# Performance work log

Hardware: AMD Instinct MI355X
Metric: run time of the kernel (lower is better)

Reference implementation:

```python
import jax, jax.numpy as jnp
import numpy as np

N, F_IN, F_OUT = 8192, 256, 256
ALPHA = 0.2  # LeakyReLU negative slope
NEG = -9e15

def setup_inputs() -> dict:
    key = jax.random.key(0)
    k1, k2, k3, k4, k5 = jax.random.split(key, 5)
    h = jax.random.normal(k1, (N, F_IN), dtype=jnp.float32)
    adj = jax.random.randint(k2, (N, N), 0, 2, dtype=jnp.int32)
    W_w = jax.random.normal(k3, (F_IN, F_OUT), dtype=jnp.float32) / np.sqrt(F_IN)
    W_b = jax.random.normal(k4, (F_OUT,), dtype=jnp.float32) * 0.01
    a = jax.random.normal(k5, (2 * F_OUT, 1), dtype=jnp.float32) / np.sqrt(2 * F_OUT)
    return {"h": h, "adj": adj, "W_w": W_w, "W_b": W_b, "a": a}

def reference(h, adj, W_w, W_b, a):
    # Wh: [N, F_OUT]
    Wh = h @ W_w + W_b
    a1 = a[:F_OUT, 0]   # scores for source node i (row)
    a2 = a[F_OUT:, 0]   # scores for target node j (col)
    # e[i,j] = leakyrelu(Wh_i . a1 + Wh_j . a2)  -- separable form of the
    # original repeat/cat construction, identical math without the NxNx2F tensor.
    e = jax.nn.leaky_relu((Wh @ a1)[:, None] + (Wh @ a2)[None, :], negative_slope=ALPHA)
    attention = jnp.where(adj > 0, e, NEG)
    attention = jax.nn.softmax(attention, axis=1)
    # dropout is identity in eval / p=0
    h_prime = attention @ Wh  # [N, F_OUT]
    return h_prime
```

## Files before the change

### kernel.cpp

```cpp
#include <hip/hip_runtime.h>
#include <stdint.h>

#define NN 8192
#define FD 256
#define LOG2E 1.44269504088896340736f
#define SPLIT 8
#define JSLICE (NN / SPLIT)
#define NIT (JSLICE / 32)

typedef __attribute__((ext_vector_type(8))) __bf16 bf16x8;
typedef __attribute__((ext_vector_type(4))) float f32x4;

__device__ __forceinline__ unsigned short f2bf(float x) {
    unsigned u = __float_as_uint(x);
    u = u + 0x7fffu + ((u >> 16) & 1u);
    return (unsigned short)(u >> 16);
}
__device__ __forceinline__ bf16x8 ld_bf8(const unsigned short* p) {
    uint4 v = *(const uint4*)p;
    return __builtin_bit_cast(bf16x8, v);
}
__device__ __forceinline__ unsigned pack_trunc2(float a, float b) {
    return __builtin_amdgcn_perm(__float_as_uint(b), __float_as_uint(a), 0x07060302u);
}
__device__ __forceinline__ void async_ld16(const void* g, void* lds) {
    __builtin_amdgcn_global_load_lds(
        (const __attribute__((address_space(1))) void*)g,
        (__attribute__((address_space(3))) void*)lds, 16, 0, 0);
}

__global__ __launch_bounds__(256) void wtrans_kernel(const float* __restrict__ W,
                                                     unsigned short* __restrict__ WbT) {
    int idx = blockIdx.x * 256 + threadIdx.x;
    int k = idx >> 8, f = idx & 255;
    WbT[f * 256 + k] = f2bf(W[idx]);
}

__global__ __launch_bounds__(256) void adjpack_kernel(const int* __restrict__ adj,
                                                      unsigned* __restrict__ adjB) {
    int t = threadIdx.x;
    int l = t & 63, w = t >> 6;
    int i = blockIdx.x * 4 + w;
    const int* arow = adj + (size_t)i * NN;
    unsigned* brow = adjB + (size_t)i * (NN / 32);
    #pragma unroll 2
    for (int c = 0; c < 32; ++c) {
        int base = c * 256;
        int v0 = arow[base + l];
        int v1 = arow[base + 64 + l];
        int v2 = arow[base + 128 + l];
        int v3 = arow[base + 192 + l];
        unsigned long long b0 = __ballot(v0 > 0);
        unsigned long long b1 = __ballot(v1 > 0);
        unsigned long long b2 = __ballot(v2 > 0);
        unsigned long long b3 = __ballot(v3 > 0);
        if (l == 0) {
            uint4 lo = make_uint4((unsigned)b0, (unsigned)(b0 >> 32),
                                  (unsigned)b1, (unsigned)(b1 >> 32));
            uint4 hi = make_uint4((unsigned)b2, (unsigned)(b2 >> 32),
                                  (unsigned)b3, (unsigned)(b3 >> 32));
            *(uint4*)(brow + c * 8) = lo;
            *(uint4*)(brow + c * 8 + 4) = hi;
        }
    }
}

__global__ __launch_bounds__(256) void btrans_kernel(const unsigned* __restrict__ rm,
                                                     unsigned* __restrict__ tm) {
    __shared__ unsigned tile[64 * 65];
    int t = threadIdx.x;
    int l = t & 63, r0 = t >> 6;
    int i0 = (blockIdx.x & 127) * 64;
    int w0 = (blockIdx.x >> 7) * 64;
    #pragma unroll
    for (int k = 0; k < 16; ++k) {
        int r = k * 4 + r0;
        tile[r * 65 + l] = rm[(size_t)(i0 + r) * (NN / 32) + w0 + l];
    }
    __syncthreads();
    #pragma unroll
    for (int k = 0; k < 16; ++k) {
        int wi = k * 4 + r0;
        tm[(size_t)(w0 + wi) * NN + i0 + l] = tile[l * 65 + wi];
    }
}

__global__ __launch_bounds__(256) void gemm1_kernel(const float* __restrict__ h,
                                                    const unsigned short* __restrict__ WbT,
                                                    const float* __restrict__ bias,
                                                    const float* __restrict__ av,
                                                    unsigned short* __restrict__ PBu,
                                                    float* __restrict__ f1p,
                                                    float* __restrict__ f2p) {
    __shared__ float Wh_s[256 * 33];
    __shared__ float red_s[2 * 8 * 32];
    int t = threadIdx.x;
    int l = t & 63, w = t >> 6;
    int i0 = blockIdx.x * 32;
    int fbase = w * 64;
    int cl = l & 15, q = l >> 4;

    f32x4 acc[2][4] = {};
    const float* hA0 = h + (size_t)(i0 + cl) * FD;
    const float* hA1 = h + (size_t)(i0 + 16 + cl) * FD;

    #pragma unroll
    for (int ks = 0; ks < 8; ++ks) {
        int kk = ks * 32 + q * 8;
        union { unsigned short u[8]; bf16x8 v; } ua0, ua1;
        float4 x0 = *(const float4*)(hA0 + kk);
        float4 x1 = *(const float4*)(hA0 + kk + 4);
        float4 y0 = *(const float4*)(hA1 + kk);
        float4 y1 = *(const float4*)(hA1 + kk + 4);
        ua0.u[0]=f2bf(x0.x); ua0.u[1]=f2bf(x0.y); ua0.u[2]=f2bf(x0.z); ua0.u[3]=f2bf(x0.w);
        ua0.u[4]=f2bf(x1.x); ua0.u[5]=f2bf(x1.y); ua0.u[6]=f2bf(x1.z); ua0.u[7]=f2bf(x1.w);
        ua1.u[0]=f2bf(y0.x); ua1.u[1]=f2bf(y0.y); ua1.u[2]=f2bf(y0.z); ua1.u[3]=f2bf(y0.w);
        ua1.u[4]=f2bf(y1.x); ua1.u[5]=f2bf(y1.y); ua1.u[6]=f2bf(y1.z); ua1.u[7]=f2bf(y1.w);
        #pragma unroll
        for (int bg = 0; bg < 4; ++bg) {
            bf16x8 bF = ld_bf8(WbT + (fbase + bg * 16 + cl) * 256 + kk);
            acc[0][bg] = __builtin_amdgcn_mfma_f32_16x16x32_bf16(ua0.v, bF, acc[0][bg], 0, 0, 0);
            acc[1][bg] = __builtin_amdgcn_mfma_f32_16x16x32_bf16(ua1.v, bF, acc[1][bg], 0, 0, 0);
        }
    }

    #pragma unroll
    for (int mt = 0; mt < 2; ++mt)
        #pragma unroll
        for (int bg = 0; bg < 4; ++bg)
            #pragma unroll
            for (int e = 0; e < 4; ++e) {
                int il = mt * 16 + q * 4 + e;
                int fl = fbase + bg * 16 + cl;
                Wh_s[fl * 33 + il] = acc[mt][bg][e] + bias[fl];
            }
    __syncthreads();
    {
        size_t jcBase = (size_t)blockIdx.x * 8192;
        #pragma unroll
        for (int u = 0; u < 4; ++u) {
            int fg = u * 4 + (t >> 6);
            int ll = t & 63;
            int c2 = ll & 15, q2 = ll >> 4;
            const float* src = &Wh_s[(fg * 16 + c2) * 33 + q2 * 8];
            union { unsigned short us[8]; uint4 v; } p;
            #pragma unroll
            for (int e = 0; e < 8; ++e) p.us[e] = f2bf(src[e]);
            *(uint4*)(PBu + jcBase + fg * 512 + ll * 8) = p.v;
        }
    }
    {
        int i = t & 31, fc = t >> 5;
        float s1 = 0.f, s2 = 0.f;
        #pragma unroll
        for (int fo = 0; fo < 32; ++fo) {
            int f = fc * 32 + fo;
            float wv = Wh_s[f * 33 + i];
            s1 += wv * av[f];
            s2 += wv * av[256 + f];
        }
        red_s[fc * 32 + i] = s1;
        red_s[256 + fc * 32 + i] = s2;
    }
    __syncthreads();
    if (t < 32) {
        float s = 0.f;
        #pragma unroll
        for (int fc = 0; fc < 8; ++fc) s += red_s[fc * 32 + t];
        f1p[i0 + t] = s * LOG2E;
    } else if (t < 64) {
        int i = t - 32;
        float s = 0.f;
        #pragma unroll
        for (int fc = 0; fc < 8; ++fc) s += red_s[256 + fc * 32 + i];
        f2p[i0 + i] = s * LOG2E;
    }
}

__global__ __launch_bounds__(256, 3) void gat_kernel(const unsigned* __restrict__ adjBT,
                                                     const unsigned short* __restrict__ PBu,
                                                     const float* __restrict__ f1p,
                                                     const float* __restrict__ f2p,
                                                     float* __restrict__ num,
                                                     float* __restrict__ den) {
    __shared__ __align__(16) unsigned short Bs[2][8192];
    __shared__ unsigned mask_s[NIT * 64];
    __shared__ float f2_s[JSLICE];

    int t = threadIdx.x;
    int l = t & 63, w = t >> 6;
    int s = blockIdx.x & 7;
    int strip = blockIdx.x >> 3;
    int i0b = strip * 64;
    int j0 = s * JSLICE;
    int jw0 = j0 / 32;
    int cl = l & 15, q = l >> 4;

    #pragma unroll
    for (int c = 0; c < 8; ++c) {
        int idx = c * 256 + t;
        int jt = idx >> 6, rl = idx & 63;
        mask_s[idx] = adjBT[(size_t)(jw0 + jt) * NN + i0b + rl];
    }
    *(float4*)&f2_s[t * 4] = *(const float4*)(f2p + j0 + t * 4);

    const char* pbBase = (const char*)(PBu + (size_t)jw0 * 8192);
    #pragma unroll
    for (int k = 0; k < 4; ++k)
        async_ld16(pbBase + k * 4096 + t * 16, (char*)&Bs[0][0] + k * 4096 + t * 16);

    float f1v = f1p[i0b + w * 16 + cl];

    const bf16x8 onesB = __builtin_bit_cast(bf16x8,
        make_uint4(0x3F803F80u, 0x3F803F80u, 0x3F803F80u, 0x3F803F80u));

    f32x4 acc[16] = {};
    f32x4 accR = {};

    #pragma unroll 1
    for (int g = 0; g < NIT; ++g) {
        __syncthreads();
        if (g + 1 < NIT) {
            const char* src = pbBase + (size_t)(g + 1) * 16384;
            char* dst = (char*)&Bs[(g + 1) & 1][0];
            #pragma unroll
            for (int k = 0; k < 4; ++k)
                async_ld16(src + k * 4096 + t * 16, dst + k * 4096 + t * 16);
        }
        unsigned mw = mask_s[g * 64 + w * 16 + cl];
        float4 F0 = *(const float4*)&f2_s[g * 32 + q * 8];
        float4 F1 = *(const float4*)&f2_s[g * 32 + q * 8 + 4];

        unsigned bits = mw >> (q * 8);
        float fe[8] = {F0.x, F0.y, F0.z, F0.w, F1.x, F1.y, F1.z, F1.w};
        float wv[8];
        #pragma unroll
        for (int e = 0; e < 8; ++e) {
            float sv = f1v + fe[e];
            sv = fmaxf(sv, 0.2f * sv);
            float x = __builtin_amdgcn_exp2f(sv);
            x = (bits >> e) & 1 ? x : 0.f;
            wv[e] = x;
        }
        union { unsigned uu[4]; bf16x8 v; } af;
        af.uu[0] = pack_trunc2(wv[0], wv[1]);
        af.uu[1] = pack_trunc2(wv[2], wv[3]);
        af.uu[2] = pack_trunc2(wv[4], wv[5]);
        af.uu[3] = pack_trunc2(wv[6], wv[7]);

        const unsigned short* bu = &Bs[g & 1][0] + l * 8;
        #pragma unroll
        for (int fg = 0; fg < 16; ++fg) {
            bf16x8 B = ld_bf8(bu + fg * 512);
            acc[fg] = __builtin_amdgcn_mfma_f32_16x16x32_bf16(af.v, B, acc[fg], 0, 0, 0);
        }
        accR = __builtin_amdgcn_mfma_f32_16x16x32_bf16(af.v, onesB, accR, 0, 0, 0);
    }

    if (cl == 0) {
        #pragma unroll
        for (int e = 0; e < 4; ++e)
            den[(size_t)s * NN + i0b + w * 16 + q * 4 + e] = accR[e];
    }

    float* nrow = num + (size_t)s * NN * FD;
    #pragma unroll
    for (int e = 0; e < 4; ++e) {
        int r = i0b + w * 16 + q * 4 + e;
        #pragma unroll
        for (int fg = 0; fg < 16; ++fg)
            nrow[(size_t)r * FD + fg * 16 + cl] = acc[fg][e];
    }
}

__global__ __launch_bounds__(256) void combine_kernel(const float* __restrict__ num,
                                                      const float* __restrict__ den,
                                                      float* __restrict__ out) {
    int idx = blockIdx.x * 256 + threadIdx.x;
    int i = idx >> 8;
    float nsum = 0.f, dsum = 0.f;
    #pragma unroll
    for (int s = 0; s < SPLIT; ++s) {
        nsum += num[(size_t)s * NN * FD + idx];
        dsum += den[(size_t)s * NN + i];
    }
    out[idx] = nsum / dsum;
}

extern "C" void kernel_launch(void* const* d_in, const int* in_sizes, int n_in,
                              void* d_out, int out_size, void* d_ws, size_t ws_size,
                              hipStream_t stream) {
    const float* h   = (const float*)d_in[0];
    const int*   adj = (const int*)d_in[1];
    const float* W   = (const float*)d_in[2];
    const float* b   = (const float*)d_in[3];
    const float* a   = (const float*)d_in[4];
    float* out = (float*)d_out;

    char* ws = (char*)d_ws;
    unsigned short* PBu = (unsigned short*)ws;
    unsigned short* WbT = (unsigned short*)(ws + (4u << 20));
    float* f1p = (float*)(ws + (4u << 20) + (128u << 10));
    float* f2p = f1p + NN;
    float* den = f2p + NN;
    unsigned* adjB  = (unsigned*)(ws + (8u << 20));
    unsigned* adjBT = (unsigned*)(ws + (16u << 20));
    float* num = (float*)(ws + (24u << 20));

    adjpack_kernel<<<NN / 4, 256, 0, stream>>>(adj, adjB);
    wtrans_kernel<<<256, 256, 0, stream>>>(W, WbT);
    btrans_kernel<<<512, 256, 0, stream>>>(adjB, adjBT);
    gemm1_kernel<<<256, 256, 0, stream>>>(h, WbT, b, a, PBu, f1p, f2p);
    gat_kernel<<<128 * SPLIT, 256, 0, stream>>>(adjBT, PBu, f1p, f2p, num, den);
    combine_kernel<<<NN * FD / 256, 256, 0, stream>>>(num, den, out);
}
```

Measured before the change: 460.9 us.

## Fuse adjacency bit-packing into GAT kernel with prefetched ballot masks

Removes the separate adjacency pack and bit-transpose kernels. The GAT kernel now reads the int32 adjacency rows directly, ballots them into per-iteration bitmasks, and double-buffers the masks in LDS while the next tile's adjacency loads overlap the MFMA work. It also raises the occupancy hint to 4 blocks and remaps gemm1's block index so its output chunks are produced in a different order. The intent is to drop the extra kernel launches and the intermediate bitmask traffic. The cost is that the 256MB adjacency read now sits inside the compute kernel and adds register pressure.

Measured after the change: 439.1 us. 1.05x faster.

```diff
diff --git a/kernel.cpp b/kernel.cpp
--- a/kernel.cpp
+++ b/kernel.cpp
@@ -34,55 +34,6 @@
     int idx = blockIdx.x * 256 + threadIdx.x;
     int k = idx >> 8, f = idx & 255;
     WbT[f * 256 + k] = f2bf(W[idx]);
-}
-
-__global__ __launch_bounds__(256) void adjpack_kernel(const int* __restrict__ adj,
-                                                      unsigned* __restrict__ adjB) {
-    int t = threadIdx.x;
-    int l = t & 63, w = t >> 6;
-    int i = blockIdx.x * 4 + w;
-    const int* arow = adj + (size_t)i * NN;
-    unsigned* brow = adjB + (size_t)i * (NN / 32);
-    #pragma unroll 2
-    for (int c = 0; c < 32; ++c) {
-        int base = c * 256;
-        int v0 = arow[base + l];
-        int v1 = arow[base + 64 + l];
-        int v2 = arow[base + 128 + l];
-        int v3 = arow[base + 192 + l];
-        unsigned long long b0 = __ballot(v0 > 0);
-        unsigned long long b1 = __ballot(v1 > 0);
-        unsigned long long b2 = __ballot(v2 > 0);
-        unsigned long long b3 = __ballot(v3 > 0);
-        if (l == 0) {
-            uint4 lo = make_uint4((unsigned)b0, (unsigned)(b0 >> 32),
-                                  (unsigned)b1, (unsigned)(b1 >> 32));
-            uint4 hi = make_uint4((unsigned)b2, (unsigned)(b2 >> 32),
-                                  (unsigned)b3, (unsigned)(b3 >> 32));
-            *(uint4*)(brow + c * 8) = lo;
-            *(uint4*)(brow + c * 8 + 4) = hi;
-        }
-    }
-}
-
-__global__ __launch_bounds__(256) void btrans_kernel(const unsigned* __restrict__ rm,
-                                                     unsigned* __restrict__ tm) {
-    __shared__ unsigned tile[64 * 65];
-    int t = threadIdx.x;
-    int l = t & 63, r0 = t >> 6;
-    int i0 = (blockIdx.x & 127) * 64;
-    int w0 = (blockIdx.x >> 7) * 64;
-    #pragma unroll
-    for (int k = 0; k < 16; ++k) {
-        int r = k * 4 + r0;
-        tile[r * 65 + l] = rm[(size_t)(i0 + r) * (NN / 32) + w0 + l];
-    }
-    __syncthreads();
-    #pragma unroll
-    for (int k = 0; k < 16; ++k) {
-        int wi = k * 4 + r0;
-        tm[(size_t)(w0 + wi) * NN + i0 + l] = tile[l * 65 + wi];
-    }
 }
 
 __global__ __launch_bounds__(256) void gemm1_kernel(const float* __restrict__ h,
@@ -96,7 +47,8 @@
     __shared__ float red_s[2 * 8 * 32];
     int t = threadIdx.x;
     int l = t & 63, w = t >> 6;
-    int i0 = blockIdx.x * 32;
+    int jc = (blockIdx.x & 7) * 32 + (blockIdx.x >> 3);
+    int i0 = jc * 32;
     int fbase = w * 64;
     int cl = l & 15, q = l >> 4;
 
@@ -136,7 +88,7 @@
             }
     __syncthreads();
     {
-        size_t jcBase = (size_t)blockIdx.x * 8192;
+        size_t jcBase = (size_t)jc * 8192;
         #pragma unroll
         for (int u = 0; u < 4; ++u) {
             int fg = u * 4 + (t >> 6);
@@ -177,14 +129,14 @@
     }
 }
 
-__global__ __launch_bounds__(256, 3) void gat_kernel(const unsigned* __restrict__ adjBT,
+__global__ __launch_bounds__(256, 4) void gat_kernel(const int* __restrict__ adj,
                                                      const unsigned short* __restrict__ PBu,
                                                      const float* __restrict__ f1p,
                                                      const float* __restrict__ f2p,
                                                      float* __restrict__ num,
                                                      float* __restrict__ den) {
     __shared__ __align__(16) unsigned short Bs[2][8192];
-    __shared__ unsigned mask_s[NIT * 64];
+    __shared__ unsigned mask_b[2][64];
     __shared__ float f2_s[JSLICE];
 
     int t = threadIdx.x;
@@ -196,18 +148,32 @@
     int jw0 = j0 / 32;
     int cl = l & 15, q = l >> 4;
 
-    #pragma unroll
-    for (int c = 0; c < 8; ++c) {
-        int idx = c * 256 + t;
-        int jt = idx >> 6, rl = idx & 63;
-        mask_s[idx] = adjBT[(size_t)(jw0 + jt) * NN + i0b + rl];
-    }
     *(float4*)&f2_s[t * 4] = *(const float4*)(f2p + j0 + t * 4);
 
     const char* pbBase = (const char*)(PBu + (size_t)jw0 * 8192);
     #pragma unroll
     for (int k = 0; k < 4; ++k)
         async_ld16(pbBase + k * 4096 + t * 16, (char*)&Bs[0][0] + k * 4096 + t * 16);
+
+    const int* arow = adj + (size_t)(i0b + w * 16 + (l >> 5)) * NN + j0 + (l & 31);
+    {
+        int v0 = arow[0 * 2 * NN], v1 = arow[1 * 2 * NN], v2 = arow[2 * 2 * NN], v3 = arow[3 * 2 * NN];
+        int v4 = arow[4 * 2 * NN], v5 = arow[5 * 2 * NN], v6 = arow[6 * 2 * NN], v7 = arow[7 * 2 * NN];
+        unsigned long long b0 = __ballot(v0 > 0), b1 = __ballot(v1 > 0);
+        unsigned long long b2 = __ballot(v2 > 0), b3 = __ballot(v3 > 0);
+        unsigned long long b4 = __ballot(v4 > 0), b5 = __ballot(v5 > 0);
+        unsigned long long b6 = __ballot(v6 > 0), b7 = __ballot(v7 > 0);
+        if (l == 0) {
+            *(uint2*)&mask_b[0][w * 16 + 0]  = make_uint2((unsigned)b0, (unsigned)(b0 >> 32));
+            *(uint2*)&mask_b[0][w * 16 + 2]  = make_uint2((unsigned)b1, (unsigned)(b1 >> 32));
+            *(uint2*)&mask_b[0][w * 16 + 4]  = make_uint2((unsigned)b2, (unsigned)(b2 >> 32));
+            *(uint2*)&mask_b[0][w * 16 + 6]  = make_uint2((unsigned)b3, (unsigned)(b3 >> 32));
+            *(uint2*)&mask_b[0][w * 16 + 8]  = make_uint2((unsigned)b4, (unsigned)(b4 >> 32));
+            *(uint2*)&mask_b[0][w * 16 + 10] = make_uint2((unsigned)b5, (unsigned)(b5 >> 32));
+            *(uint2*)&mask_b[0][w * 16 + 12] = make_uint2((unsigned)b6, (unsigned)(b6 >> 32));
+            *(uint2*)&mask_b[0][w * 16 + 14] = make_uint2((unsigned)b7, (unsigned)(b7 >> 32));
+        }
+    }
 
     float f1v = f1p[i0b + w * 16 + cl];
 
@@ -220,14 +186,21 @@
     #pragma unroll 1
     for (int g = 0; g < NIT; ++g) {
         __syncthreads();
+        int a0, a1, a2, a3, a4, a5, a6, a7;
         if (g + 1 < NIT) {
             const char* src = pbBase + (size_t)(g + 1) * 16384;
             char* dst = (char*)&Bs[(g + 1) & 1][0];
             #pragma unroll
             for (int k = 0; k < 4; ++k)
                 async_ld16(src + k * 4096 + t * 16, dst + k * 4096 + t * 16);
-        }
-        unsigned mw = mask_s[g * 64 + w * 16 + cl];
+            int jo = (g + 1) * 32;
+            a0 = arow[0 * 2 * NN + jo]; a1 = arow[1 * 2 * NN + jo];
+            a2 = arow[2 * 2 * NN + jo]; a3 = arow[3 * 2 * NN + jo];
+            a4 = arow[4 * 2 * NN + jo]; a5 = arow[5 * 2 * NN + jo];
+            a6 = arow[6 * 2 * NN + jo]; a7 = arow[7 * 2 * NN + jo];
+        }
+
+        unsigned mw = mask_b[g & 1][w * 16 + cl];
         float4 F0 = *(const float4*)&f2_s[g * 32 + q * 8];
         float4 F1 = *(const float4*)&f2_s[g * 32 + q * 8 + 4];
 
@@ -255,6 +228,24 @@
             acc[fg] = __builtin_amdgcn_mfma_f32_16x16x32_bf16(af.v, B, acc[fg], 0, 0, 0);
         }
         accR = __builtin_amdgcn_mfma_f32_16x16x32_bf16(af.v, onesB, accR, 0, 0, 0);
+
+        if (g + 1 < NIT) {
+            int nb = (g + 1) & 1;
+            unsigned long long b0 = __ballot(a0 > 0), b1 = __ballot(a1 > 0);
+            unsigned long long b2 = __ballot(a2 > 0), b3 = __ballot(a3 > 0);
+            unsigned long long b4 = __ballot(a4 > 0), b5 = __ballot(a5 > 0);
+            unsigned long long b6 = __ballot(a6 > 0), b7 = __ballot(a7 > 0);
+            if (l == 0) {
+                *(uint2*)&mask_b[nb][w * 16 + 0]  = make_uint2((unsigned)b0, (unsigned)(b0 >> 32));
+                *(uint2*)&mask_b[nb][w * 16 + 2]  = make_uint2((unsigned)b1, (unsigned)(b1 >> 32));
+                *(uint2*)&mask_b[nb][w * 16 + 4]  = make_uint2((unsigned)b2, (unsigned)(b2 >> 32));
+                *(uint2*)&mask_b[nb][w * 16 + 6]  = make_uint2((unsigned)b3, (unsigned)(b3 >> 32));
+                *(uint2*)&mask_b[nb][w * 16 + 8]  = make_uint2((unsigned)b4, (unsigned)(b4 >> 32));
+                *(uint2*)&mask_b[nb][w * 16 + 10] = make_uint2((unsigned)b5, (unsigned)(b5 >> 32));
+                *(uint2*)&mask_b[nb][w * 16 + 12] = make_uint2((unsigned)b6, (unsigned)(b6 >> 32));
+                *(uint2*)&mask_b[nb][w * 16 + 14] = make_uint2((unsigned)b7, (unsigned)(b7 >> 32));
+            }
+        }
     }
 
     if (cl == 0) {
@@ -303,14 +294,10 @@
     float* f1p = (float*)(ws + (4u << 20) + (128u << 10));
     float* f2p = f1p + NN;
     float* den = f2p + NN;
-    unsigned* adjB  = (unsigned*)(ws + (8u << 20));
-    unsigned* adjBT = (unsigned*)(ws + (16u << 20));
     float* num = (float*)(ws + (24u << 20));
 
-    adjpack_kernel<<<NN / 4, 256, 0, stream>>>(adj, adjB);
     wtrans_kernel<<<256, 256, 0, stream>>>(W, WbT);
-    btrans_kernel<<<512, 256, 0, stream>>>(adjB, adjBT);
     gemm1_kernel<<<256, 256, 0, stream>>>(h, WbT, b, a, PBu, f1p, f2p);
-    gat_kernel<<<128 * SPLIT, 256, 0, stream>>>(adjBT, PBu, f1p, f2p, num, den);
+    gat_kernel<<<128 * SPLIT, 256, 0, stream>>>(adj, PBu, f1p, f2p, num, den);
     combine_kernel<<<NN * FD / 256, 256, 0, stream>>>(num, den, out);
 }
```
